# Kernel optimization log

Hardware: AMD Instinct MI355X
Metric: run time of the kernel (lower is better)

## Reference

```python
import jax, jax.numpy as jnp
import numpy as np

N, HW, ENC = 128, 14, 2048
V, E, D = 10000, 512, 512
MAXLEN = 32


def setup_inputs() -> dict:
    key = jax.random.key(0)
    ks = jax.random.split(key, 16)
    s = 0.02
    enc_feature = jax.random.normal(ks[0], (N, HW, HW, ENC), jnp.float32)
    enc_capt = jax.random.randint(ks[1], (N, MAXLEN), 0, V)
    capt_lengths = jax.random.randint(ks[2], (N, 1), 2, MAXLEN + 1)
    capt_lengths = capt_lengths.at[0, 0].set(MAXLEN)  # ensure max(decode_lengths)==MAXLEN-1 (static)
    rn = lambda k, sh: jax.random.normal(k, sh, jnp.float32) * s
    return dict(
        enc_feature=enc_feature, enc_capt=enc_capt, capt_lengths=capt_lengths,
        emb=rn(ks[3], (V, E)),
        W_ih=rn(ks[4], (4 * D, E + ENC)), b_ih=jnp.zeros((4 * D,), jnp.float32),
        W_hh=rn(ks[5], (4 * D, D)), b_hh=jnp.zeros((4 * D,), jnp.float32),
        W_inith=rn(ks[6], (D, ENC)), b_inith=jnp.zeros((D,), jnp.float32),
        W_initc=rn(ks[7], (D, ENC)), b_initc=jnp.zeros((D,), jnp.float32),
        W_fbeta=rn(ks[8], (ENC, D)), b_fbeta=jnp.zeros((ENC,), jnp.float32),
        W_fc=rn(ks[9], (V, D)), b_fc=jnp.zeros((V,), jnp.float32),
    )


def reference(enc_feature, enc_capt, capt_lengths, emb, W_ih, b_ih, W_hh, b_hh,
              W_inith, b_inith, W_initc, b_initc, W_fbeta, b_fbeta, W_fc, b_fc):
    n = enc_feature.shape[0]
    feat = enc_feature.reshape(n, -1, enc_feature.shape[-1])  # (N, P, ENC)
    P = feat.shape[1]
    cl = capt_lengths[:, 0]
    sort_ind = jnp.argsort(-cl)               # descending by caption length
    cl = cl[sort_ind]
    feat = feat[sort_ind]
    capt = enc_capt[sort_ind]
    embs = emb[capt]                          # (N, MAXLEN, E)
    mean_feat = feat.mean(axis=1)             # (N, ENC) - uniform attention context
    h = mean_feat @ W_inith.T + b_inith
    c = mean_feat @ W_initc.T + b_initc
    dec_len = cl - 1
    T = capt.shape[1] - 1                     # static max decode length
    mask = jnp.arange(T)[None, :] < dec_len[:, None]   # (N, T) ragged-batch mask
    xs = (jnp.swapaxes(embs[:, :T, :], 0, 1), mask.T)  # (T,N,E), (T,N)

    def step(carry, x):
        h, c = carry
        e_t, m = x
        gate = jax.nn.sigmoid(h @ W_fbeta.T + b_fbeta)          # (N, ENC)
        awe = mean_feat * gate                                   # gated attention-weighted encoding
        inp = jnp.concatenate([e_t, awe], axis=1)                # (N, E+ENC)
        g = inp @ W_ih.T + b_ih + h @ W_hh.T + b_hh              # LSTMCell gates
        i, f, gg, o = jnp.split(g, 4, axis=1)
        c_new = jax.nn.sigmoid(f) * c + jax.nn.sigmoid(i) * jnp.tanh(gg)
        h_new = jax.nn.sigmoid(o) * jnp.tanh(c_new)
        mf = m[:, None].astype(h.dtype)
        h2 = jnp.where(m[:, None], h_new, h)                     # inactive rows keep old state
        c2 = jnp.where(m[:, None], c_new, c)
        preds = (h_new @ W_fc.T + b_fc) * mf                     # dropout = identity (eval)
        return (h2, c2), (preds, mf)

    (_, _), (preds, mfs) = jax.lax.scan(step, (h, c), xs)
    predictions = jnp.swapaxes(preds, 0, 1)                      # (N, T, V)
    alphas = jnp.broadcast_to(jnp.swapaxes(mfs, 0, 1) / P, (n, T, P))  # uniform alpha, zero past len
    return predictions, capt, dec_len, alphas, sort_ind
```

## Files before the change

### kernel.cpp

```cpp
#include <hip/hip_runtime.h>
#include <hip/hip_bf16.h>
#include <math.h>

#define NB       128
#define P_HW     196
#define ENC_C    2048
#define V_SZ     10000
#define E_SZ     512
#define D_SZ     512
#define MAXLEN   32
#define T_STEPS  31

#define SZ_PRED    (128ULL * 31ULL * 10000ULL)
#define OFF_PRED   0ULL
#define OFF_CAPT   (SZ_PRED)
#define OFF_DECLEN (OFF_CAPT + 128ULL * 32ULL)
#define OFF_ALPHA  (OFF_DECLEN + 128ULL)
#define OFF_SORT   (OFF_ALPHA + 128ULL * 31ULL * 196ULL)

typedef __bf16 bf16x8 __attribute__((ext_vector_type(8)));
typedef float f32x4 __attribute__((ext_vector_type(4)));

__device__ __forceinline__ float sigf(float x) { return 1.0f / (1.0f + __expf(-x)); }

__device__ __forceinline__ unsigned short f2bf(float f) {
    unsigned int u = __float_as_uint(f);
    unsigned int r = (u + 0x7fffu + ((u >> 16) & 1u)) >> 16;
    return (unsigned short)r;
}

__global__ void sort_kernel(const int* __restrict__ capt_lengths,
                            const int* __restrict__ enc_capt,
                            int* __restrict__ sort_ind_ws,
                            int* __restrict__ dec_len_ws,
                            int* __restrict__ capt_sorted_ws,
                            float* __restrict__ dout) {
    __shared__ int cl[NB];
    int i = threadIdx.x;
    cl[i] = capt_lengths[i];
    __syncthreads();
    int my = cl[i];
    int rank = 0;
    #pragma unroll 4
    for (int j = 0; j < NB; ++j) {
        int cj = cl[j];
        rank += (cj > my) || (cj == my && j < i);
    }
    sort_ind_ws[rank] = i;
    dec_len_ws[rank]  = my - 1;
    dout[OFF_SORT + rank]   = (float)i;
    dout[OFF_DECLEN + rank] = (float)(my - 1);
    for (int t = 0; t < MAXLEN; ++t) {
        int tok = enc_capt[i * MAXLEN + t];
        capt_sorted_ws[rank * MAXLEN + t] = tok;
        dout[OFF_CAPT + rank * MAXLEN + t] = (float)tok;
    }
}

__global__ void mean_kernel(const float* __restrict__ enc_feature,
                            const int* __restrict__ sort_ind,
                            float* __restrict__ mean_feat,
                            unsigned short* __restrict__ mean16) {
    int b = blockIdx.y;
    int e = blockIdx.x * 256 + threadIdx.x;
    int src = sort_ind[b];
    const float* base = enc_feature + (size_t)src * P_HW * ENC_C + e;
    float s = 0.0f;
    #pragma unroll 4
    for (int p = 0; p < P_HW; ++p) s += base[(size_t)p * ENC_C];
    float m = s * (1.0f / (float)P_HW);
    mean_feat[(size_t)b * ENC_C + e] = m;
    mean16[(size_t)b * ENC_C + e] = f2bf(m);
}

__global__ void f32_to_bf16(const float* __restrict__ src,
                            unsigned short* __restrict__ dst, int n) {
    int i = (blockIdx.x * 256 + threadIdx.x) * 4;
    if (i < n) {
        float4 v = *reinterpret_cast<const float4*>(src + i);
        dst[i + 0] = f2bf(v.x);
        dst[i + 1] = f2bf(v.y);
        dst[i + 2] = f2bf(v.z);
        dst[i + 3] = f2bf(v.w);
    }
}

__global__ void concat_wg(const float* __restrict__ W_ih,
                          const float* __restrict__ W_hh,
                          unsigned short* __restrict__ Wg16) {
    int n = blockIdx.y;
    int col = blockIdx.x * 256 + threadIdx.x;
    float v = (col < 2560) ? W_ih[(size_t)n * 2560 + col]
                           : W_hh[(size_t)n * 512 + (col - 2560)];
    Wg16[(size_t)n * 3072 + col] = f2bf(v);
}

__global__ void bsum_kernel(const float* __restrict__ b_ih,
                            const float* __restrict__ b_hh,
                            float* __restrict__ bsum) {
    int i = blockIdx.x * 256 + threadIdx.x;
    bsum[i] = b_ih[i] + b_hh[i];
}

__global__ void embs_gather(const float* __restrict__ emb,
                            const int* __restrict__ capt_sorted,
                            unsigned short* __restrict__ embs16) {
    int idx = blockIdx.x * 256 + threadIdx.x;
    if (idx >= 31 * 128 * 512) return;
    int t = idx >> 16;
    int r = idx & 65535;
    int b = r >> 9;
    int tok = capt_sorted[b * MAXLEN + t];
    embs16[idx] = f2bf(emb[(size_t)tok * E_SZ + (r & 511)]);
}

template <int EPI>
__global__ __launch_bounds__(64) void mfma_gemm(
    const unsigned short* __restrict__ A, int lda,
    const unsigned short* __restrict__ B, int ldb,
    int Nout, int K,
    const float* __restrict__ bias,
    float* __restrict__ Cf, unsigned short* __restrict__ Cb, int ldc) {
    int l = threadIdx.x;
    int lm = l & 15;
    int lk = (l >> 4) << 3;
    int row0 = blockIdx.y << 5;
    int col0 = blockIdx.x << 5;
    const unsigned short* pa0 = A + (size_t)(row0 + lm) * lda + lk;
    const unsigned short* pa1 = pa0 + ((size_t)lda << 4);
    const unsigned short* pb0 = B + (size_t)(col0 + lm) * ldb + lk;
    const unsigned short* pb1 = pb0 + ((size_t)ldb << 4);
    f32x4 acc00 = {0.f, 0.f, 0.f, 0.f}, acc01 = acc00, acc10 = acc00, acc11 = acc00;
    for (int k = 0; k < K; k += 32) {
        bf16x8 a0 = *(const bf16x8*)(pa0 + k);
        bf16x8 a1 = *(const bf16x8*)(pa1 + k);
        bf16x8 b0 = *(const bf16x8*)(pb0 + k);
        bf16x8 b1 = *(const bf16x8*)(pb1 + k);
        acc00 = __builtin_amdgcn_mfma_f32_16x16x32_bf16(a0, b0, acc00, 0, 0, 0);
        acc01 = __builtin_amdgcn_mfma_f32_16x16x32_bf16(a0, b1, acc01, 0, 0, 0);
        acc10 = __builtin_amdgcn_mfma_f32_16x16x32_bf16(a1, b0, acc10, 0, 0, 0);
        acc11 = __builtin_amdgcn_mfma_f32_16x16x32_bf16(a1, b1, acc11, 0, 0, 0);
    }
    int orow = (l >> 4) << 2;
    #pragma unroll
    for (int mi = 0; mi < 2; ++mi) {
        #pragma unroll
        for (int ni = 0; ni < 2; ++ni) {
            f32x4 v = (mi == 0) ? (ni == 0 ? acc00 : acc01)
                                : (ni == 0 ? acc10 : acc11);
            int col = col0 + ni * 16 + lm;
            #pragma unroll
            for (int r = 0; r < 4; ++r) {
                int row = row0 + mi * 16 + orow + r;
                float val = v[r] + bias[col];
                if (EPI == 0) Cf[(size_t)row * ldc + col] = val;
                else          Cb[(size_t)row * ldc + col] = f2bf(val);
            }
        }
    }
}

__global__ __launch_bounds__(256) void awe_fused(
    const unsigned short* __restrict__ h16,
    const unsigned short* __restrict__ Wfb,
    const float* __restrict__ b_fbeta,
    const float* __restrict__ meanfeat,
    unsigned short* __restrict__ awe16) {
    __shared__ float red[2][1024];
    int tid = threadIdx.x;
    int w = tid >> 6, l = tid & 63;
    int ct = w >> 1, ks = w & 1;
    int lm = l & 15, lk = ((l >> 4) << 3);
    int row0 = blockIdx.y << 5;
    int col0 = (blockIdx.x << 6) + (ct << 5);
    int kbase = ks << 8;
    const unsigned short* pa0 = h16 + (size_t)(row0 + lm) * 512 + kbase + lk;
    const unsigned short* pa1 = pa0 + 16 * 512;
    const unsigned short* pb0 = Wfb + (size_t)(col0 + lm) * 512 + kbase + lk;
    const unsigned short* pb1 = pb0 + 16 * 512;
    f32x4 acc00 = {0.f, 0.f, 0.f, 0.f}, acc01 = acc00, acc10 = acc00, acc11 = acc00;
    #pragma unroll
    for (int k = 0; k < 256; k += 32) {
        bf16x8 a0 = *(const bf16x8*)(pa0 + k);
        bf16x8 a1 = *(const bf16x8*)(pa1 + k);
        bf16x8 b0 = *(const bf16x8*)(pb0 + k);
        bf16x8 b1 = *(const bf16x8*)(pb1 + k);
        acc00 = __builtin_amdgcn_mfma_f32_16x16x32_bf16(a0, b0, acc00, 0, 0, 0);
        acc01 = __builtin_amdgcn_mfma_f32_16x16x32_bf16(a0, b1, acc01, 0, 0, 0);
        acc10 = __builtin_amdgcn_mfma_f32_16x16x32_bf16(a1, b0, acc10, 0, 0, 0);
        acc11 = __builtin_amdgcn_mfma_f32_16x16x32_bf16(a1, b1, acc11, 0, 0, 0);
    }
    int orow = (l >> 4) << 2;
    if (ks == 1) {
        #pragma unroll
        for (int mi = 0; mi < 2; ++mi)
            #pragma unroll
            for (int ni = 0; ni < 2; ++ni) {
                f32x4 v = (mi == 0) ? (ni == 0 ? acc00 : acc01)
                                    : (ni == 0 ? acc10 : acc11);
                #pragma unroll
                for (int r = 0; r < 4; ++r)
                    red[ct][(mi * 16 + orow + r) * 32 + ni * 16 + lm] = v[r];
            }
    }
    __syncthreads();
    if (ks == 0) {
        #pragma unroll
        for (int mi = 0; mi < 2; ++mi)
            #pragma unroll
            for (int ni = 0; ni < 2; ++ni) {
                f32x4 v = (mi == 0) ? (ni == 0 ? acc00 : acc01)
                                    : (ni == 0 ? acc10 : acc11);
                int col = col0 + ni * 16 + lm;
                #pragma unroll
                for (int r = 0; r < 4; ++r) {
                    int row = row0 + mi * 16 + orow + r;
                    float val = v[r] + red[ct][(mi * 16 + orow + r) * 32 + ni * 16 + lm]
                              + b_fbeta[col];
                    awe16[(size_t)row * 2048 + col] =
                        f2bf(meanfeat[(size_t)row * 2048 + col] * sigf(val));
                }
            }
    }
}

__global__ __launch_bounds__(1024) void lstm_fused(
    const unsigned short* __restrict__ embt,
    const unsigned short* __restrict__ awe16,
    const unsigned short* __restrict__ h16,
    const unsigned short* __restrict__ Wg,
    const float* __restrict__ bsum,
    float* __restrict__ c,
    unsigned short* __restrict__ h16out,
    unsigned short* __restrict__ hnew16,
    const int* __restrict__ dec_len, int t) {
    __shared__ float red[12][1024];
    __shared__ float gates[4][1024];
    int tid = threadIdx.x;
    int w = tid >> 6, l = tid & 63;
    int g = w & 3, ks = w >> 2;
    int lm = l & 15, lk = ((l >> 4) << 3);
    int row0 = blockIdx.y << 5;
    int d0 = blockIdx.x << 5;
    int r0 = row0 + lm;
    const unsigned short* pe0 = embt + (size_t)r0 * 512 + lk;
    const unsigned short* pe1 = pe0 + 16 * 512;
    const unsigned short* pw0 = awe16 + (size_t)r0 * 2048 + lk;
    const unsigned short* pw1 = pw0 + 16 * 2048;
    const unsigned short* ph0 = h16 + (size_t)r0 * 512 + lk;
    const unsigned short* ph1 = ph0 + 16 * 512;
    const unsigned short* pb0 = Wg + (size_t)(g * 512 + d0 + lm) * 3072 + lk;
    const unsigned short* pb1 = pb0 + (size_t)16 * 3072;
    f32x4 acc00 = {0.f, 0.f, 0.f, 0.f}, acc01 = acc00, acc10 = acc00, acc11 = acc00;
    int k0 = ks * 768;
    #pragma unroll 4
    for (int kk = 0; kk < 768; kk += 32) {
        int k = k0 + kk;
        bf16x8 a0, a1;
        if (k < 512)       { a0 = *(const bf16x8*)(pe0 + k);
                             a1 = *(const bf16x8*)(pe1 + k); }
        else if (k < 2560) { a0 = *(const bf16x8*)(pw0 + (k - 512));
                             a1 = *(const bf16x8*)(pw1 + (k - 512)); }
        else               { a0 = *(const bf16x8*)(ph0 + (k - 2560));
                             a1 = *(const bf16x8*)(ph1 + (k - 2560)); }
        bf16x8 b0 = *(const bf16x8*)(pb0 + k);
        bf16x8 b1 = *(const bf16x8*)(pb1 + k);
        acc00 = __builtin_amdgcn_mfma_f32_16x16x32_bf16(a0, b0, acc00, 0, 0, 0);
        acc01 = __builtin_amdgcn_mfma_f32_16x16x32_bf16(a0, b1, acc01, 0, 0, 0);
        acc10 = __builtin_amdgcn_mfma_f32_16x16x32_bf16(a1, b0, acc10, 0, 0, 0);
        acc11 = __builtin_amdgcn_mfma_f32_16x16x32_bf16(a1, b1, acc11, 0, 0, 0);
    }
    int orow = (l >> 4) << 2;
    if (ks > 0) {
        int slot = (ks - 1) * 4 + g;
        #pragma unroll
        for (int mi = 0; mi < 2; ++mi)
            #pragma unroll
            for (int ni = 0; ni < 2; ++ni) {
                f32x4 v = (mi == 0) ? (ni == 0 ? acc00 : acc01)
                                    : (ni == 0 ? acc10 : acc11);
                #pragma unroll
                for (int r = 0; r < 4; ++r)
                    red[slot][(mi * 16 + orow + r) * 32 + ni * 16 + lm] = v[r];
            }
    }
    __syncthreads();
    if (ks == 0) {
        #pragma unroll
        for (int mi = 0; mi < 2; ++mi)
            #pragma unroll
            for (int ni = 0; ni < 2; ++ni) {
                f32x4 v = (mi == 0) ? (ni == 0 ? acc00 : acc01)
                                    : (ni == 0 ? acc10 : acc11);
                #pragma unroll
                for (int r = 0; r < 4; ++r) {
                    int idx = (mi * 16 + orow + r) * 32 + ni * 16 + lm;
                    gates[g][idx] = v[r] + red[g][idx] + red[4 + g][idx] + red[8 + g][idx];
                }
            }
    }
    __syncthreads();
    {
        int row = tid >> 5, d = tid & 31;
        int R = row0 + row, D = d0 + d;
        int e = row * 32 + d;
        float gi = gates[0][e] + bsum[D];
        float gf = gates[1][e] + bsum[512 + D];
        float gg = gates[2][e] + bsum[1024 + D];
        float go = gates[3][e] + bsum[1536 + D];
        size_t idx = (size_t)R * 512 + D;
        float cn = sigf(gf) * c[idx] + sigf(gi) * tanhf(gg);
        float hn = sigf(go) * tanhf(cn);
        hnew16[idx] = f2bf(hn);
        if (t < dec_len[R]) {
            c[idx] = cn;
            h16out[idx] = f2bf(hn);
        }
    }
}

__global__ __launch_bounds__(256) void fc_batched(
    const unsigned short* __restrict__ hnew_all,
    const unsigned short* __restrict__ Wfc,
    const float* __restrict__ b_fc,
    const int* __restrict__ dec_len,
    float* __restrict__ out) {
    int tid = threadIdx.x;
    int w = tid >> 6, l = tid & 63;
    int mi2 = w >> 1, ni2 = w & 1;
    int lm = l & 15, lk = ((l >> 4) << 3);
    int row0 = blockIdx.y * 64 + mi2 * 32;
    int col0 = blockIdx.x * 64 + ni2 * 32;
    const unsigned short* pa0 = hnew_all + (size_t)(row0 + lm) * 512 + lk;
    const unsigned short* pa1 = pa0 + 16 * 512;
    int bn0 = col0 + lm; if (bn0 > 9999) bn0 = 9999;
    int bn1 = col0 + 16 + lm; if (bn1 > 9999) bn1 = 9999;
    const unsigned short* pb0 = Wfc + (size_t)bn0 * 512 + lk;
    const unsigned short* pb1 = Wfc + (size_t)bn1 * 512 + lk;
    f32x4 acc00 = {0.f, 0.f, 0.f, 0.f}, acc01 = acc00, acc10 = acc00, acc11 = acc00;
    #pragma unroll 4
    for (int k = 0; k < 512; k += 32) {
        bf16x8 a0 = *(const bf16x8*)(pa0 + k);
        bf16x8 a1 = *(const bf16x8*)(pa1 + k);
        bf16x8 b0 = *(const bf16x8*)(pb0 + k);
        bf16x8 b1 = *(const bf16x8*)(pb1 + k);
        acc00 = __builtin_amdgcn_mfma_f32_16x16x32_bf16(a0, b0, acc00, 0, 0, 0);
        acc01 = __builtin_amdgcn_mfma_f32_16x16x32_bf16(a0, b1, acc01, 0, 0, 0);
        acc10 = __builtin_amdgcn_mfma_f32_16x16x32_bf16(a1, b0, acc10, 0, 0, 0);
        acc11 = __builtin_amdgcn_mfma_f32_16x16x32_bf16(a1, b1, acc11, 0, 0, 0);
    }
    int orow = (l >> 4) << 2;
    #pragma unroll
    for (int mi = 0; mi < 2; ++mi)
        #pragma unroll
        for (int ni = 0; ni < 2; ++ni) {
            f32x4 v = (mi == 0) ? (ni == 0 ? acc00 : acc01)
                                : (ni == 0 ? acc10 : acc11);
            int col = col0 + ni * 16 + lm;
            if (col >= 10000) continue;
            #pragma unroll
            for (int r = 0; r < 4; ++r) {
                int row = row0 + mi * 16 + orow + r;
                int t = row >> 7, b = row & 127;
                float val = v[r] + b_fc[col];
                bool m = t < dec_len[b];
                out[OFF_PRED + ((size_t)b * 31 + t) * 10000 + col] = m ? val : 0.0f;
            }
        }
}

__global__ void alphas_kernel(const int* __restrict__ dec_len,
                              float* __restrict__ dout) {
    int idx = blockIdx.x * 256 + threadIdx.x;
    int b = idx / (31 * 196);
    int r = idx % (31 * 196);
    int t = r / 196;
    dout[OFF_ALPHA + idx] = (t < dec_len[b]) ? (1.0f / 196.0f) : 0.0f;
}

static inline char* align256(char* p) {
    return (char*)(((uintptr_t)p + 255) & ~(uintptr_t)255);
}

extern "C" void kernel_launch(void* const* d_in, const int* in_sizes, int n_in,
                              void* d_out, int out_size, void* d_ws, size_t ws_size,
                              hipStream_t stream) {
    const float* enc_feature  = (const float*)d_in[0];
    const int*   enc_capt     = (const int*)d_in[1];
    const int*   capt_lengths = (const int*)d_in[2];
    const float* emb     = (const float*)d_in[3];
    const float* W_ih    = (const float*)d_in[4];
    const float* b_ih    = (const float*)d_in[5];
    const float* W_hh    = (const float*)d_in[6];
    const float* b_hh    = (const float*)d_in[7];
    const float* W_inith = (const float*)d_in[8];
    const float* b_inith = (const float*)d_in[9];
    const float* W_initc = (const float*)d_in[10];
    const float* b_initc = (const float*)d_in[11];
    const float* W_fbeta = (const float*)d_in[12];
    const float* b_fbeta = (const float*)d_in[13];
    const float* W_fc    = (const float*)d_in[14];
    const float* b_fc    = (const float*)d_in[15];
    float* out = (float*)d_out;

    char* ws = (char*)d_ws;
    int* sort_ind    = (int*)ws;  ws += 512;
    int* dec_len     = (int*)ws;  ws += 512;
    int* capt_sorted = (int*)ws;  ws += 128 * MAXLEN * sizeof(int);
    ws = align256(ws);
    float* mean_feat = (float*)ws; ws += (size_t)128 * 2048 * 4;
    float* c         = (float*)ws; ws += (size_t)128 * 512 * 4;
    float* bsum      = (float*)ws; ws += 2048 * 4;
    unsigned short* mean16   = (unsigned short*)ws; ws += (size_t)128 * 2048 * 2;
    unsigned short* h16      = (unsigned short*)ws; ws += (size_t)128 * 512 * 2;
    unsigned short* awe16    = (unsigned short*)ws; ws += (size_t)128 * 2048 * 2;
    unsigned short* Wfb16    = (unsigned short*)ws; ws += (size_t)2048 * 512 * 2;
    unsigned short* Wg16     = (unsigned short*)ws; ws += (size_t)2048 * 3072 * 2;
    unsigned short* Wfc16    = (unsigned short*)ws; ws += (size_t)10000 * 512 * 2;
    unsigned short* Winith16 = (unsigned short*)ws; ws += (size_t)512 * 2048 * 2;
    unsigned short* Winitc16 = (unsigned short*)ws; ws += (size_t)512 * 2048 * 2;
    unsigned short* embs16   = (unsigned short*)ws; ws += (size_t)31 * 128 * 512 * 2;
    unsigned short* hnew_all = (unsigned short*)ws; ws += (size_t)31 * 128 * 512 * 2;

    sort_kernel<<<1, 128, 0, stream>>>(capt_lengths, enc_capt, sort_ind, dec_len,
                                       capt_sorted, out);
    mean_kernel<<<dim3(8, 128), 256, 0, stream>>>(enc_feature, sort_ind,
                                                  mean_feat, mean16);

    f32_to_bf16<<<(2048 * 512 / 4 + 255) / 256, 256, 0, stream>>>(W_fbeta, Wfb16, 2048 * 512);
    f32_to_bf16<<<(10000 * 512 / 4 + 255) / 256, 256, 0, stream>>>(W_fc, Wfc16, 10000 * 512);
    f32_to_bf16<<<(512 * 2048 / 4 + 255) / 256, 256, 0, stream>>>(W_inith, Winith16, 512 * 2048);
    f32_to_bf16<<<(512 * 2048 / 4 + 255) / 256, 256, 0, stream>>>(W_initc, Winitc16, 512 * 2048);
    concat_wg<<<dim3(12, 2048), 256, 0, stream>>>(W_ih, W_hh, Wg16);
    bsum_kernel<<<8, 256, 0, stream>>>(b_ih, b_hh, bsum);
    embs_gather<<<(31 * 128 * 512 + 255) / 256, 256, 0, stream>>>(emb, capt_sorted, embs16);

    mfma_gemm<4><<<dim3(16, 4), 64, 0, stream>>>(
        mean16, 2048, Winith16, 2048, 512, 2048, b_inith, nullptr, h16, 512);
    mfma_gemm<0><<<dim3(16, 4), 64, 0, stream>>>(
        mean16, 2048, Winitc16, 2048, 512, 2048, b_initc, c, nullptr, 512);

    for (int t = 0; t < T_STEPS; ++t) {
        awe_fused<<<dim3(32, 4), 256, 0, stream>>>(
            h16, Wfb16, b_fbeta, mean_feat, awe16);
        lstm_fused<<<dim3(16, 4), 1024, 0, stream>>>(
            embs16 + (size_t)t * 128 * 512, awe16, h16, Wg16, bsum,
            c, h16, hnew_all + (size_t)t * 128 * 512, dec_len, t);
    }

    fc_batched<<<dim3(157, 62), 256, 0, stream>>>(
        hnew_all, Wfc16, b_fc, dec_len, out);
    alphas_kernel<<<3038, 256, 0, stream>>>(dec_len, out);
}
```

Baseline: 2.341 ms.

## Double-buffer LSTM hidden state, halve LSTM tile width, enlarge FC tile

The LSTM step kernel now computes 16 hidden columns per block instead of 32, doubling the grid to 128 blocks so more compute units work during each recurrent step. Gate reduction reuses the partial-sum shared buffer, so the separate gates array is gone. The hidden state is ping-ponged between two buffers, which removes the read/write race on h across blocks, and inactive rows copy their old h forward. The final vocabulary projection uses 128x128 block tiles with a 4x4 MFMA register tile per wave to reuse more operands from registers, at the cost of higher register pressure.

```diff
diff --git a/kernel.cpp b/kernel.cpp
--- a/kernel.cpp
+++ b/kernel.cpp
@@ -224,36 +224,34 @@
     }
 }
 
-__global__ __launch_bounds__(1024) void lstm_fused(
+__global__ __launch_bounds__(1024) void lstm_fused2(
     const unsigned short* __restrict__ embt,
     const unsigned short* __restrict__ awe16,
-    const unsigned short* __restrict__ h16,
+    const unsigned short* __restrict__ h_in,
     const unsigned short* __restrict__ Wg,
     const float* __restrict__ bsum,
     float* __restrict__ c,
-    unsigned short* __restrict__ h16out,
+    unsigned short* __restrict__ h_out,
     unsigned short* __restrict__ hnew16,
     const int* __restrict__ dec_len, int t) {
-    __shared__ float red[12][1024];
-    __shared__ float gates[4][1024];
+    __shared__ float red[12][512];
     int tid = threadIdx.x;
     int w = tid >> 6, l = tid & 63;
     int g = w & 3, ks = w >> 2;
     int lm = l & 15, lk = ((l >> 4) << 3);
-    int row0 = blockIdx.y << 5;
-    int d0 = blockIdx.x << 5;
-    int r0 = row0 + lm;
-    const unsigned short* pe0 = embt + (size_t)r0 * 512 + lk;
+    int r0 = blockIdx.y << 5;
+    int d0 = blockIdx.x << 4;
+    int ra = r0 + lm;
+    const unsigned short* pe0 = embt  + (size_t)ra * 512  + lk;
     const unsigned short* pe1 = pe0 + 16 * 512;
-    const unsigned short* pw0 = awe16 + (size_t)r0 * 2048 + lk;
+    const unsigned short* pw0 = awe16 + (size_t)ra * 2048 + lk;
     const unsigned short* pw1 = pw0 + 16 * 2048;
-    const unsigned short* ph0 = h16 + (size_t)r0 * 512 + lk;
+    const unsigned short* ph0 = h_in  + (size_t)ra * 512  + lk;
     const unsigned short* ph1 = ph0 + 16 * 512;
-    const unsigned short* pb0 = Wg + (size_t)(g * 512 + d0 + lm) * 3072 + lk;
-    const unsigned short* pb1 = pb0 + (size_t)16 * 3072;
-    f32x4 acc00 = {0.f, 0.f, 0.f, 0.f}, acc01 = acc00, acc10 = acc00, acc11 = acc00;
+    const unsigned short* pb  = Wg + (size_t)(g * 512 + d0 + lm) * 3072 + lk;
+    f32x4 acc0 = {0.f, 0.f, 0.f, 0.f}, acc1 = acc0;
     int k0 = ks * 768;
-    #pragma unroll 4
+    #pragma unroll 8
     for (int kk = 0; kk < 768; kk += 32) {
         int k = k0 + kk;
         bf16x8 a0, a1;
@@ -263,63 +261,53 @@
                              a1 = *(const bf16x8*)(pw1 + (k - 512)); }
         else               { a0 = *(const bf16x8*)(ph0 + (k - 2560));
                              a1 = *(const bf16x8*)(ph1 + (k - 2560)); }
-        bf16x8 b0 = *(const bf16x8*)(pb0 + k);
-        bf16x8 b1 = *(const bf16x8*)(pb1 + k);
-        acc00 = __builtin_amdgcn_mfma_f32_16x16x32_bf16(a0, b0, acc00, 0, 0, 0);
-        acc01 = __builtin_amdgcn_mfma_f32_16x16x32_bf16(a0, b1, acc01, 0, 0, 0);
-        acc10 = __builtin_amdgcn_mfma_f32_16x16x32_bf16(a1, b0, acc10, 0, 0, 0);
-        acc11 = __builtin_amdgcn_mfma_f32_16x16x32_bf16(a1, b1, acc11, 0, 0, 0);
+        bf16x8 b = *(const bf16x8*)(pb + k);
+        acc0 = __builtin_amdgcn_mfma_f32_16x16x32_bf16(a0, b, acc0, 0, 0, 0);
+        acc1 = __builtin_amdgcn_mfma_f32_16x16x32_bf16(a1, b, acc1, 0, 0, 0);
     }
     int orow = (l >> 4) << 2;
     if (ks > 0) {
         int slot = (ks - 1) * 4 + g;
         #pragma unroll
-        for (int mi = 0; mi < 2; ++mi)
-            #pragma unroll
-            for (int ni = 0; ni < 2; ++ni) {
-                f32x4 v = (mi == 0) ? (ni == 0 ? acc00 : acc01)
-                                    : (ni == 0 ? acc10 : acc11);
-                #pragma unroll
-                for (int r = 0; r < 4; ++r)
-                    red[slot][(mi * 16 + orow + r) * 32 + ni * 16 + lm] = v[r];
-            }
+        for (int r = 0; r < 4; ++r) {
+            red[slot][(orow + r) * 16 + lm]      = acc0[r];
+            red[slot][(16 + orow + r) * 16 + lm] = acc1[r];
+        }
     }
     __syncthreads();
     if (ks == 0) {
         #pragma unroll
-        for (int mi = 0; mi < 2; ++mi)
-            #pragma unroll
-            for (int ni = 0; ni < 2; ++ni) {
-                f32x4 v = (mi == 0) ? (ni == 0 ? acc00 : acc01)
-                                    : (ni == 0 ? acc10 : acc11);
-                #pragma unroll
-                for (int r = 0; r < 4; ++r) {
-                    int idx = (mi * 16 + orow + r) * 32 + ni * 16 + lm;
-                    gates[g][idx] = v[r] + red[g][idx] + red[4 + g][idx] + red[8 + g][idx];
-                }
-            }
+        for (int r = 0; r < 4; ++r) {
+            int e0 = (orow + r) * 16 + lm;
+            int e1 = (16 + orow + r) * 16 + lm;
+            red[g][e0] = acc0[r] + red[g][e0] + red[4 + g][e0] + red[8 + g][e0];
+            red[g][e1] = acc1[r] + red[g][e1] + red[4 + g][e1] + red[8 + g][e1];
+        }
     }
     __syncthreads();
-    {
-        int row = tid >> 5, d = tid & 31;
-        int R = row0 + row, D = d0 + d;
-        int e = row * 32 + d;
-        float gi = gates[0][e] + bsum[D];
-        float gf = gates[1][e] + bsum[512 + D];
-        float gg = gates[2][e] + bsum[1024 + D];
-        float go = gates[3][e] + bsum[1536 + D];
+    if (tid < 512) {
+        int r = tid >> 4, d = tid & 15;
+        int R = r0 + r, D = d0 + d;
+        int e = r * 16 + d;
+        float gi = red[0][e] + bsum[D];
+        float gf = red[1][e] + bsum[512 + D];
+        float gg = red[2][e] + bsum[1024 + D];
+        float go = red[3][e] + bsum[1536 + D];
         size_t idx = (size_t)R * 512 + D;
         float cn = sigf(gf) * c[idx] + sigf(gi) * tanhf(gg);
         float hn = sigf(go) * tanhf(cn);
-        hnew16[idx] = f2bf(hn);
+        unsigned short hb = f2bf(hn);
+        hnew16[idx] = hb;
         if (t < dec_len[R]) {
             c[idx] = cn;
-            h16out[idx] = f2bf(hn);
+            h_out[idx] = hb;
+        } else {
+            h_out[idx] = h_in[idx];
         }
     }
 }
 
-__global__ __launch_bounds__(256) void fc_batched(
+__global__ __launch_bounds__(256) void fc128(
     const unsigned short* __restrict__ hnew_all,
     const unsigned short* __restrict__ Wfc,
     const float* __restrict__ b_fc,
@@ -327,46 +315,53 @@
     float* __restrict__ out) {
     int tid = threadIdx.x;
     int w = tid >> 6, l = tid & 63;
-    int mi2 = w >> 1, ni2 = w & 1;
+    int wm = w >> 1, wn = w & 1;
     int lm = l & 15, lk = ((l >> 4) << 3);
-    int row0 = blockIdx.y * 64 + mi2 * 32;
-    int col0 = blockIdx.x * 64 + ni2 * 32;
-    const unsigned short* pa0 = hnew_all + (size_t)(row0 + lm) * 512 + lk;
-    const unsigned short* pa1 = pa0 + 16 * 512;
-    int bn0 = col0 + lm; if (bn0 > 9999) bn0 = 9999;
-    int bn1 = col0 + 16 + lm; if (bn1 > 9999) bn1 = 9999;
-    const unsigned short* pb0 = Wfc + (size_t)bn0 * 512 + lk;
-    const unsigned short* pb1 = Wfc + (size_t)bn1 * 512 + lk;
-    f32x4 acc00 = {0.f, 0.f, 0.f, 0.f}, acc01 = acc00, acc10 = acc00, acc11 = acc00;
-    #pragma unroll 4
+    int row0 = blockIdx.x * 128 + wm * 64;
+    int col0 = blockIdx.y * 128 + wn * 64;
+    const unsigned short* pa[4];
+    const unsigned short* pb[4];
+    #pragma unroll
+    for (int i = 0; i < 4; ++i) {
+        pa[i] = hnew_all + (size_t)(row0 + i * 16 + lm) * 512 + lk;
+        int bn = col0 + i * 16 + lm; if (bn > 9999) bn = 9999;
+        pb[i] = Wfc + (size_t)bn * 512 + lk;
+    }
+    f32x4 acc[4][4];
+    #pragma unroll
+    for (int i = 0; i < 4; ++i)
+        #pragma unroll
+        for (int j = 0; j < 4; ++j) acc[i][j] = (f32x4){0.f, 0.f, 0.f, 0.f};
     for (int k = 0; k < 512; k += 32) {
-        bf16x8 a0 = *(const bf16x8*)(pa0 + k);
-        bf16x8 a1 = *(const bf16x8*)(pa1 + k);
-        bf16x8 b0 = *(const bf16x8*)(pb0 + k);
-        bf16x8 b1 = *(const bf16x8*)(pb1 + k);
-        acc00 = __builtin_amdgcn_mfma_f32_16x16x32_bf16(a0, b0, acc00, 0, 0, 0);
-        acc01 = __builtin_amdgcn_mfma_f32_16x16x32_bf16(a0, b1, acc01, 0, 0, 0);
-        acc10 = __builtin_amdgcn_mfma_f32_16x16x32_bf16(a1, b0, acc10, 0, 0, 0);
-        acc11 = __builtin_amdgcn_mfma_f32_16x16x32_bf16(a1, b1, acc11, 0, 0, 0);
+        bf16x8 a[4], b[4];
+        #pragma unroll
+        for (int i = 0; i < 4; ++i) a[i] = *(const bf16x8*)(pa[i] + k);
+        #pragma unroll
+        for (int j = 0; j < 4; ++j) b[j] = *(const bf16x8*)(pb[j] + k);
+        #pragma unroll
+        for (int i = 0; i < 4; ++i)
+            #pragma unroll
+            for (int j = 0; j < 4; ++j)
+                acc[i][j] = __builtin_amdgcn_mfma_f32_16x16x32_bf16(a[i], b[j], acc[i][j], 0, 0, 0);
     }
     int orow = (l >> 4) << 2;
     #pragma unroll
-    for (int mi = 0; mi < 2; ++mi)
-        #pragma unroll
-        for (int ni = 0; ni < 2; ++ni) {
-            f32x4 v = (mi == 0) ? (ni == 0 ? acc00 : acc01)
-                                : (ni == 0 ? acc10 : acc11);
-            int col = col0 + ni * 16 + lm;
+    for (int i = 0; i < 4; ++i) {
+        #pragma unroll
+        for (int j = 0; j < 4; ++j) {
+            int col = col0 + j * 16 + lm;
             if (col >= 10000) continue;
+            float bias = b_fc[col];
             #pragma unroll
             for (int r = 0; r < 4; ++r) {
-                int row = row0 + mi * 16 + orow + r;
+                int row = row0 + i * 16 + orow + r;
                 int t = row >> 7, b = row & 127;
-                float val = v[r] + b_fc[col];
                 bool m = t < dec_len[b];
-                out[OFF_PRED + ((size_t)b * 31 + t) * 10000 + col] = m ? val : 0.0f;
+                out[OFF_PRED + ((size_t)b * 31 + t) * 10000 + col] =
+                    m ? (acc[i][j][r] + bias) : 0.0f;
             }
         }
+    }
 }
 
 __global__ void alphas_kernel(const int* __restrict__ dec_len,
@@ -412,7 +407,8 @@
     float* c         = (float*)ws; ws += (size_t)128 * 512 * 4;
     float* bsum      = (float*)ws; ws += 2048 * 4;
     unsigned short* mean16   = (unsigned short*)ws; ws += (size_t)128 * 2048 * 2;
-    unsigned short* h16      = (unsigned short*)ws; ws += (size_t)128 * 512 * 2;
+    unsigned short* hbuf0    = (unsigned short*)ws; ws += (size_t)128 * 512 * 2;
+    unsigned short* hbuf1    = (unsigned short*)ws; ws += (size_t)128 * 512 * 2;
     unsigned short* awe16    = (unsigned short*)ws; ws += (size_t)128 * 2048 * 2;
     unsigned short* Wfb16    = (unsigned short*)ws; ws += (size_t)2048 * 512 * 2;
     unsigned short* Wg16     = (unsigned short*)ws; ws += (size_t)2048 * 3072 * 2;
@@ -436,19 +432,22 @@
     embs_gather<<<(31 * 128 * 512 + 255) / 256, 256, 0, stream>>>(emb, capt_sorted, embs16);
 
     mfma_gemm<4><<<dim3(16, 4), 64, 0, stream>>>(
-        mean16, 2048, Winith16, 2048, 512, 2048, b_inith, nullptr, h16, 512);
+        mean16, 2048, Winith16, 2048, 512, 2048, b_inith, nullptr, hbuf0, 512);
     mfma_gemm<0><<<dim3(16, 4), 64, 0, stream>>>(
         mean16, 2048, Winitc16, 2048, 512, 2048, b_initc, c, nullptr, 512);
 
+    unsigned short* hb[2] = {hbuf0, hbuf1};
     for (int t = 0; t < T_STEPS; ++t) {
+        unsigned short* hin  = hb[t & 1];
+        unsigned short* hout = hb[(t + 1) & 1];
         awe_fused<<<dim3(32, 4), 256, 0, stream>>>(
-            h16, Wfb16, b_fbeta, mean_feat, awe16);
-        lstm_fused<<<dim3(16, 4), 1024, 0, stream>>>(
-            embs16 + (size_t)t * 128 * 512, awe16, h16, Wg16, bsum,
-            c, h16, hnew_all + (size_t)t * 128 * 512, dec_len, t);
-    }
-
-    fc_batched<<<dim3(157, 62), 256, 0, stream>>>(
+            hin, Wfb16, b_fbeta, mean_feat, awe16);
+        lstm_fused2<<<dim3(32, 4), 1024, 0, stream>>>(
+            embs16 + (size_t)t * 128 * 512, awe16, hin, Wg16, bsum,
+            c, hout, hnew_all + (size_t)t * 128 * 512, dec_len, t);
+    }
+
+    fc128<<<dim3(31, 79), 256, 0, stream>>>(
         hnew_all, Wfc16, b_fc, dec_len, out);
     alphas_kernel<<<3038, 256, 0, stream>>>(dec_len, out);
 }
```

Result: faster. 1.907 ms (-18.5%).
